# Kernel tuning notes

Measured on AMD Instinct MI355X. Metric: run time of the kernel, lower is better.

The kernel has to match this reference:

```python
import jax, jax.numpy as jnp
import numpy as np

B, T, D = 2, 2048, 2048
H, HKV = 16, 16
SEM, GEO = 1024, 1024
DH = D // H          # 128, v head dim
DS = SEM // H        # 64, sem head dim
DG = GEO // H        # 64, geo head dim (== rope_dim)
ROPE_BASE = 10000.0


def _split_heads(x, n_heads, hd):
    b, t, _ = x.shape
    return x.reshape(b, t, n_heads, hd).transpose(0, 2, 1, 3)  # (B,H,T,hd)


def _rope(x, pos_offset):
    # x: (B,H,T,DG); rotate-half RoPE over the full geo head dim
    b, h, t, d = x.shape
    inv_freq = 1.0 / (ROPE_BASE ** (jnp.arange(0, d, 2, dtype=jnp.float32) / d))
    pos = jnp.arange(t, dtype=jnp.float32) + jnp.float32(pos_offset)
    ang = pos[:, None] * inv_freq[None, :]            # (T, d/2)
    cos, sin = jnp.cos(ang), jnp.sin(ang)             # (T, d/2)
    x1, x2 = x[..., : d // 2], x[..., d // 2 :]
    return jnp.concatenate([x1 * cos - x2 * sin, x2 * cos + x1 * sin], axis=-1)


def setup_inputs() -> dict:
    key = jax.random.key(0)
    ks = jax.random.split(key, 8)
    s = lambda fan_in: 1.0 / np.sqrt(fan_in)
    return {
        "x": jax.random.normal(ks[0], (B, T, D), dtype=jnp.float32),
        "Wq_sem": jax.random.normal(ks[1], (D, SEM), dtype=jnp.float32) * s(D),
        "Wk_sem": jax.random.normal(ks[2], (D, SEM), dtype=jnp.float32) * s(D),
        "Wq_geo": jax.random.normal(ks[3], (D, GEO), dtype=jnp.float32) * s(D),
        "Wk_geo": jax.random.normal(ks[4], (D, GEO), dtype=jnp.float32) * s(D),
        "Wv": jax.random.normal(ks[5], (D, D), dtype=jnp.float32) * s(D),
        "Wo": jax.random.normal(ks[6], (D, D), dtype=jnp.float32) * s(D),
        "gate_logit": jax.random.normal(ks[7], (H,), dtype=jnp.float32) * 0.1,
        "pos_offset": 0,
    }


def reference(x, Wq_sem, Wk_sem, Wq_geo, Wk_geo, Wv, Wo, gate_logit, pos_offset):
    qsh = _split_heads(x @ Wq_sem, H, DS)    # (B,H,T,DS)
    ksh = _split_heads(x @ Wk_sem, HKV, DS)
    qgh = _split_heads(x @ Wq_geo, H, DG)    # (B,H,T,DG)
    kgh = _split_heads(x @ Wk_geo, HKV, DG)
    vh = _split_heads(x @ Wv, HKV, DH)       # (B,H,T,DH)

    qgh = _rope(qgh, pos_offset)
    kgh = _rope(kgh, pos_offset)

    gate = jax.nn.sigmoid(gate_logit).reshape(1, H, 1, 1).astype(x.dtype)
    qsh = qsh * (2.0 * gate)
    qgh = qgh * (2.0 - 2.0 * gate)

    sem_scale = 1.0 / np.sqrt(float(DS))
    geo_scale = 1.0 / np.sqrt(float(DG))
    # decoupled logits: sem and geo contributions each with their own scale
    logits = (jnp.einsum("bhqd,bhkd->bhqk", qsh, ksh) * sem_scale
              + jnp.einsum("bhqd,bhkd->bhqk", qgh, kgh) * geo_scale)

    t = x.shape[1]
    causal = jnp.tril(jnp.ones((t, t), dtype=bool))
    logits = jnp.where(causal, logits, jnp.finfo(logits.dtype).min)
    attn = jax.nn.softmax(logits, axis=-1)

    out_h = jnp.einsum("bhqk,bhkd->bhqd", attn, vh)   # (B,H,T,DH)
    out = out_h.transpose(0, 2, 1, 3).reshape(x.shape[0], t, H * DH)
    return out @ Wo
```

## Files before the change

### kernel.cpp

```cpp
#include <hip/hip_runtime.h>
#include <hip/hip_bf16.h>
#include <math.h>

#define B_ 2
#define T_ 2048
#define D_ 2048
#define H_ 16
#define DH_ 128
#define SEM_ 1024
#define GEO_ 1024
#define NPROJ 6144

typedef unsigned short ushort_t;
typedef short bf16x8 __attribute__((ext_vector_type(8)));
typedef float f32x4 __attribute__((ext_vector_type(4)));
typedef unsigned short us4 __attribute__((ext_vector_type(4)));

static __device__ inline ushort_t f2b(float x) {
    __hip_bfloat16 h = __float2bfloat16(x);
    return *reinterpret_cast<ushort_t*>(&h);
}
static __device__ inline float b2f(ushort_t u) {
    union { unsigned int i; float f; } v; v.i = ((unsigned int)u) << 16; return v.f;
}
static __device__ inline void gload_lds16(const ushort_t* g, ushort_t* l) {
    __builtin_amdgcn_global_load_lds(
        (const __attribute__((address_space(1))) void*)g,
        (__attribute__((address_space(3))) void*)l, 16, 0, 0);
}

__global__ __launch_bounds__(256) void convert_x(
    const float* __restrict__ x, ushort_t* __restrict__ xh)
{
    size_t i = ((size_t)blockIdx.x * 256 + threadIdx.x) * 8;
    float4 a = *(const float4*)&x[i];
    float4 b = *(const float4*)&x[i + 4];
    bf16x8 o;
    o[0] = (short)f2b(a.x); o[1] = (short)f2b(a.y);
    o[2] = (short)f2b(a.z); o[3] = (short)f2b(a.w);
    o[4] = (short)f2b(b.x); o[5] = (short)f2b(b.y);
    o[6] = (short)f2b(b.z); o[7] = (short)f2b(b.w);
    *(bf16x8*)&xh[i] = o;
}

__global__ __launch_bounds__(256) void transpose_all(
    const float* __restrict__ W0, const float* __restrict__ W1,
    const float* __restrict__ W2, const float* __restrict__ W3,
    const float* __restrict__ W4, const float* __restrict__ W5,
    ushort_t* __restrict__ Wt_all, ushort_t* __restrict__ WoT)
{
    const int z = blockIdx.z;
    const float* W;
    ushort_t* dst;
    int N;
    switch (z) {
        case 0: W = W0; dst = Wt_all;                          N = 1024; break;
        case 1: W = W1; dst = Wt_all + (size_t)1024 * 2048;    N = 1024; break;
        case 2: W = W2; dst = Wt_all + (size_t)2048 * 2048;    N = 1024; break;
        case 3: W = W3; dst = Wt_all + (size_t)3072 * 2048;    N = 1024; break;
        case 4: W = W4; dst = Wt_all + (size_t)4096 * 2048;    N = 2048; break;
        default: W = W5; dst = WoT;                            N = 2048; break;
    }
    const int n0 = blockIdx.x * 32;
    if (n0 >= N) return;
    const int k0 = blockIdx.y * 32;

    __shared__ float tile[32][33];
    const int c = threadIdx.x & 31, r = threadIdx.x >> 5;
#pragma unroll
    for (int rr = 0; rr < 32; rr += 8)
        tile[r + rr][c] = W[(size_t)(k0 + r + rr) * N + n0 + c];
    __syncthreads();
#pragma unroll
    for (int rr = 0; rr < 32; rr += 8)
        dst[(size_t)(n0 + r + rr) * 2048 + k0 + c] = f2b(tile[c][r + rr]);
}

#define BARS()  { asm volatile("" ::: "memory"); __builtin_amdgcn_s_barrier(); asm volatile("" ::: "memory"); }
#define WL0()   asm volatile("s_waitcnt lgkmcnt(0)" ::: "memory")
#define WV6()   asm volatile("s_waitcnt vmcnt(6)" ::: "memory")

#define LDA8(par, iq, i4, kk) \
    (*(const bf16x8*)&smA[(par)*16384 + (iq)*8192 + aoff + (i4)*1024 + ((kk) ? ca1 : ca0)])
#define LDB8(par, jq, j1, kk) \
    (*(const bf16x8*)&smB[(par)*16384 + (jq)*8192 + boff + (j1)*2048 + ((kk) ? ca1 : ca0)])

#define READ_A(par, iq) \
    aF[0]=LDA8(par,iq,0,0); aF[1]=LDA8(par,iq,0,1); \
    aF[2]=LDA8(par,iq,1,0); aF[3]=LDA8(par,iq,1,1); \
    aF[4]=LDA8(par,iq,2,0); aF[5]=LDA8(par,iq,2,1); \
    aF[6]=LDA8(par,iq,3,0); aF[7]=LDA8(par,iq,3,1);

#define READ_B(par, jq) \
    bF[(jq)*4+0]=LDB8(par,jq,0,0); bF[(jq)*4+1]=LDB8(par,jq,0,1); \
    bF[(jq)*4+2]=LDB8(par,jq,1,0); bF[(jq)*4+3]=LDB8(par,jq,1,1);

#define STAGE_A(h, kt, par) do { \
    const ushort_t* _s = gAbase + (size_t)((h)*128) * 2048 + (kt)*64 + stgoff; \
    ushort_t* _d = smA + (par)*16384 + (h)*8192 + wid*512; \
    gload_lds16(_s, _d); \
    gload_lds16(_s + (size_t)64*2048, _d + 4096); \
} while(0)

#define STAGE_B(h, kt, par) do { \
    const ushort_t* _s = gBbase + (size_t)((h)*128) * 2048 + (kt)*64 + stgoff; \
    ushort_t* _d = smB + (par)*16384 + (h)*8192 + wid*512; \
    gload_lds16(_s, _d); \
    gload_lds16(_s + (size_t)64*2048, _d + 4096); \
} while(0)

#define MM16(iq, jq) do { \
    _Pragma("unroll") \
    for (int i4 = 0; i4 < 4; ++i4) { \
        acc[(iq)*4+i4][(jq)*2+0] = __builtin_amdgcn_mfma_f32_16x16x32_bf16(aF[i4*2+0], bF[(jq)*4+0], acc[(iq)*4+i4][(jq)*2+0], 0, 0, 0); \
        acc[(iq)*4+i4][(jq)*2+0] = __builtin_amdgcn_mfma_f32_16x16x32_bf16(aF[i4*2+1], bF[(jq)*4+1], acc[(iq)*4+i4][(jq)*2+0], 0, 0, 0); \
        acc[(iq)*4+i4][(jq)*2+1] = __builtin_amdgcn_mfma_f32_16x16x32_bf16(aF[i4*2+0], bF[(jq)*4+2], acc[(iq)*4+i4][(jq)*2+1], 0, 0, 0); \
        acc[(iq)*4+i4][(jq)*2+1] = __builtin_amdgcn_mfma_f32_16x16x32_bf16(aF[i4*2+1], bF[(jq)*4+3], acc[(iq)*4+i4][(jq)*2+1], 0, 0, 0); \
    } \
} while(0)

#define TILE_BODY(par, parn, kt1, kt2) \
    STAGE_A(1, kt1, parn); \
    BARS(); WL0(); \
    __builtin_amdgcn_s_setprio(1); MM16(0, 0); __builtin_amdgcn_s_setprio(0); \
    READ_B(par, 1); \
    BARS(); \
    STAGE_A(0, kt2, par); \
    BARS(); WL0(); \
    __builtin_amdgcn_s_setprio(1); MM16(0, 1); __builtin_amdgcn_s_setprio(0); \
    READ_A(par, 1); \
    BARS(); \
    STAGE_B(0, kt2, par); \
    BARS(); WL0(); \
    __builtin_amdgcn_s_setprio(1); MM16(1, 1); __builtin_amdgcn_s_setprio(0); \
    BARS(); \
    STAGE_B(1, kt2, par); WV6(); \
    BARS(); \
    __builtin_amdgcn_s_setprio(1); MM16(1, 0); __builtin_amdgcn_s_setprio(0); \
    READ_A(parn, 0); READ_B(parn, 0); \
    BARS();

__global__ __launch_bounds__(512, 2) void gemm_proj(
    const ushort_t* __restrict__ A, const ushort_t* __restrict__ Bt,
    const float* __restrict__ gate_logit, const int* __restrict__ pos_off,
    ushort_t* __restrict__ Qh, ushort_t* __restrict__ Kh,
    ushort_t* __restrict__ Vt)
{
    extern __shared__ __align__(16) ushort_t smdyn[];
    ushort_t* smA = smdyn;
    ushort_t* smB = smdyn + 32768;

    const int tid  = threadIdx.x;
    const int wid  = tid >> 6, lane = tid & 63;
    const int ln16 = lane & 15, g = lane >> 4;
    const int wm = wid & 1, wn = wid >> 1;

    const int lin = blockIdx.y * 24 + blockIdx.x;
    const int swz = (lin & 7) * 48 + (lin >> 3);
    const int m0 = (swz / 24) * 256, n0 = (swz % 24) * 256;

    const int srow = wid * 8 + (lane >> 3);
    const int scol = ((lane & 7) ^ (lane >> 3)) * 8;
    const size_t stgoff = (size_t)srow * 2048 + scol;
    const ushort_t* gAbase = A  + (size_t)m0 * 2048;
    const ushort_t* gBbase = Bt + (size_t)n0 * 2048;

    const int cg0 = ln16 & 7;
    const int ca0 = ((g + 0) ^ cg0) * 8;
    const int ca1 = ((g + 4) ^ cg0) * 8;
    const int aoff = wm * 4096 + ln16 * 64;
    const int boff = (wn >> 1) * 4096 + (wn & 1) * 1024 + ln16 * 64;

    f32x4 acc[8][4];
#pragma unroll
    for (int i = 0; i < 8; ++i)
#pragma unroll
        for (int j = 0; j < 4; ++j) acc[i][j] = (f32x4){0.f, 0.f, 0.f, 0.f};
    bf16x8 aF[8], bF[8];

    STAGE_A(0, 0, 0); STAGE_B(0, 0, 0); STAGE_B(1, 0, 0); STAGE_A(1, 0, 0);
    STAGE_A(0, 1, 1); STAGE_B(0, 1, 1); STAGE_B(1, 1, 1);
    WV6();
    BARS();
    READ_A(0, 0); READ_B(0, 0);

#pragma unroll 1
    for (int t = 0; t < 32; t += 2) {
        const int ka1 = t + 1;
        const int ka2 = (t + 2 < 32) ? t + 2 : 31;
        const int kb1 = ka2;
        const int kb2 = (t + 3 < 32) ? t + 3 : 31;
        TILE_BODY(0, 1, ka1, ka2);
        TILE_BODY(1, 0, kb1, kb2);
    }
    asm volatile("s_waitcnt vmcnt(0) lgkmcnt(0)" ::: "memory");

    const int region = n0 >> 10;
    const int rbase  = m0 + wm * 64 + g * 4;

    if (region <= 1) {
        ushort_t* dst = (region == 0) ? Qh : Kh;
        const int hb  = ((n0 & 1023) >> 6) + (wn >> 1);
        const int d64 = (wn & 1) * 16 + ln16;
        float sc0 = 1.0f, sc1 = 1.0f;
        if (region == 0) {
            sc0 = 0.25f / (1.0f + __expf(-gate_logit[hb]));
            sc1 = 0.25f / (1.0f + __expf(-gate_logit[hb + 2]));
        }
#pragma unroll
        for (int i = 0; i < 8; ++i)
#pragma unroll
            for (int r = 0; r < 4; ++r) {
                int row = rbase + (i >> 2) * 128 + (i & 3) * 16 + r;
                int t = row & (T_ - 1), bb = row >> 11;
                size_t b0 = ((size_t)(bb * H_ + hb)     * T_ + t) * 128;
                size_t b1 = ((size_t)(bb * H_ + hb + 2) * T_ + t) * 128;
                dst[b0 + d64]      = f2b(acc[i][0][r] * sc0);
                dst[b0 + d64 + 32] = f2b(acc[i][1][r] * sc0);
                dst[b1 + d64]      = f2b(acc[i][2][r] * sc1);
                dst[b1 + d64 + 32] = f2b(acc[i][3][r] * sc1);
            }
    } else if (region <= 3) {
        ushort_t* dst = (region == 2) ? Qh : Kh;
        const int hb = ((n0 & 1023) >> 6) + (wn >> 1);
        const int ip = (wn & 1) * 16 + ln16;
        const float invf = __expf(-0.28782313665087625f * (float)ip);
        const float po = (float)(*pos_off);
        float sc0 = 1.0f, sc1 = 1.0f;
        if (region == 2) {
            sc0 = 0.25f * (1.0f - 1.0f / (1.0f + __expf(-gate_logit[hb])));
            sc1 = 0.25f * (1.0f - 1.0f / (1.0f + __expf(-gate_logit[hb + 2])));
        }
#pragma unroll
        for (int i = 0; i < 8; ++i)
#pragma unroll
            for (int r = 0; r < 4; ++r) {
                int row = rbase + (i >> 2) * 128 + (i & 3) * 16 + r;
                int t = row & (T_ - 1), bb = row >> 11;
                float s, c;
                __sincosf(((float)t + po) * invf, &s, &c);
                size_t b0 = ((size_t)(bb * H_ + hb)     * T_ + t) * 128;
                size_t b1 = ((size_t)(bb * H_ + hb + 2) * T_ + t) * 128;
                float x1 = acc[i][0][r], x2 = acc[i][1][r];
                dst[b0 + 64 + ip] = f2b((x1 * c - x2 * s) * sc0);
                dst[b0 + 96 + ip] = f2b((x2 * c + x1 * s) * sc0);
                x1 = acc[i][2][r]; x2 = acc[i][3][r];
                dst[b1 + 64 + ip] = f2b((x1 * c - x2 * s) * sc1);
                dst[b1 + 96 + ip] = f2b((x2 * c + x1 * s) * sc1);
            }
    } else {
        const int hb = (n0 - 4096) >> 7;
        const int db = (wn >> 1) * 64 + (wn & 1) * 16 + ln16;
#pragma unroll
        for (int i = 0; i < 8; ++i) {
            int row0 = rbase + (i >> 2) * 128 + (i & 3) * 16;
            int t0 = row0 & (T_ - 1), bb = row0 >> 11;
#pragma unroll
            for (int j = 0; j < 4; ++j) {
                us4 v;
                v[0] = f2b(acc[i][j][0]); v[1] = f2b(acc[i][j][1]);
                v[2] = f2b(acc[i][j][2]); v[3] = f2b(acc[i][j][3]);
                int hh = hb + (j >> 1);
                int dd = db + (j & 1) * 32;
                *(us4*)&Vt[((size_t)(bb * H_ + hh) * DH_ + dd) * T_ + t0] = v;
            }
        }
    }
}

__global__ __launch_bounds__(256) void gemm_bt_f32(
    const ushort_t* __restrict__ A, const ushort_t* __restrict__ Bt,
    float* __restrict__ C, int M, int N, int K)
{
    __shared__ ushort_t As[128 * 32];
    __shared__ ushort_t Bs[128 * 32];

    const int tid  = threadIdx.x;
    const int wid  = tid >> 6, lane = tid & 63;
    const int ln16 = lane & 15, g = lane >> 4;
    const int wm = wid & 1, wn = wid >> 1;
    const int m0 = blockIdx.y * 128, n0 = blockIdx.x * 128;

    const int lrow = lane >> 2;
    const int lc8  = (lane & 3) * 8;
    const ushort_t* gA = A  + (size_t)(m0 + wid * 32 + lrow) * K + lc8;
    const ushort_t* gB = Bt + (size_t)(n0 + wid * 32 + lrow) * K + lc8;
    ushort_t* lA = As + wid * 1024;
    ushort_t* lB = Bs + wid * 1024;
    const size_t K16 = (size_t)16 * K;

    f32x4 acc[4][4];
#pragma unroll
    for (int i = 0; i < 4; ++i)
#pragma unroll
        for (int j = 0; j < 4; ++j) acc[i][j] = (f32x4){0.f, 0.f, 0.f, 0.f};

    for (int k0 = 0; k0 < K; k0 += 32) {
        __syncthreads();
        gload_lds16(gA,       lA);
        gload_lds16(gA + K16, lA + 512);
        gload_lds16(gB,       lB);
        gload_lds16(gB + K16, lB + 512);
        gA += 32; gB += 32;
        __syncthreads();

        bf16x8 af[4], bfr[4];
#pragma unroll
        for (int i = 0; i < 4; ++i)
            af[i] = *(const bf16x8*)&As[(wm * 64 + i * 16 + ln16) * 32 + g * 8];
#pragma unroll
        for (int j = 0; j < 4; ++j)
            bfr[j] = *(const bf16x8*)&Bs[(wn * 64 + j * 16 + ln16) * 32 + g * 8];
#pragma unroll
        for (int i = 0; i < 4; ++i)
#pragma unroll
            for (int j = 0; j < 4; ++j)
                acc[i][j] = __builtin_amdgcn_mfma_f32_16x16x32_bf16(
                    af[i], bfr[j], acc[i][j], 0, 0, 0);
    }

#pragma unroll
    for (int i = 0; i < 4; ++i)
#pragma unroll
        for (int j = 0; j < 4; ++j)
#pragma unroll
            for (int r = 0; r < 4; ++r) {
                int row = m0 + wm * 64 + i * 16 + g * 4 + r;
                int col = n0 + wn * 64 + j * 16 + ln16;
                C[(size_t)row * N + col] = acc[i][j][r];
            }
}

#define P_PITCH  40

__global__ __launch_bounds__(256) void flash_attn(
    const ushort_t* __restrict__ Qh,
    const ushort_t* __restrict__ Kh,
    const ushort_t* __restrict__ Vt,
    ushort_t* __restrict__ aoh)
{
    __shared__ ushort_t Ks[32 * 128];
    __shared__ ushort_t Vs[128 * 32];
    __shared__ ushort_t Pl[4 * 16 * P_PITCH];

    const int tid  = threadIdx.x;
    const int wid  = tid >> 6, lane = tid & 63;
    const int ln16 = lane & 15, g = lane >> 4;
    const int p    = blockIdx.x;
    const int h  = blockIdx.y, b = blockIdx.z;
    const int bh = b * H_ + h;

    const ushort_t* Kbase = Kh + (size_t)bh * T_ * 128;
    const ushort_t* Vbase = Vt + (size_t)bh * 128 * T_;
    ushort_t* Pw = Pl + wid * 16 * P_PITCH;

    const int sk0 = tid,      sk1 = 256 + tid;
    const int kr0 = sk0 >> 4, kc0 = sk0 & 15;
    const int kr1 = sk1 >> 4, kc1 = sk1 & 15;
    const int vd0 = sk0 >> 2, vg0 = sk0 & 3;
    const int vd1 = sk1 >> 2, vg1 = sk1 & 3;
    const int kofs0 = (kc0 ^ (kr0 & 15)) * 8, kofs1 = (kc1 ^ (kr1 & 15)) * 8;
    const int vofs0 = (vg0 ^ ((vd0 + (vd0 >> 2)) & 3)) * 8;
    const int vofs1 = (vg1 ^ ((vd1 + (vd1 >> 2)) & 3)) * 8;

    bf16x8 bones;
    {
        short o = (ln16 == 0) ? (short)0x3F80 : (short)0;
#pragma unroll
        for (int j = 0; j < 8; ++j) bones[j] = o;
    }

#pragma unroll 1
    for (int ti = 0; ti < 2; ++ti) {
        const int qt = ti ? (31 - p) : p;
        const int q0 = qt * 64;
        const int qw = q0 + wid * 16;

        bf16x8 aq[4];
        {
            const ushort_t* qrow = Qh + ((size_t)bh * T_ + qw + ln16) * 128;
#pragma unroll
            for (int c2 = 0; c2 < 4; ++c2)
                aq[c2] = *(const bf16x8*)(qrow + c2 * 32 + g * 8);
        }

        f32x4 acc[8];
#pragma unroll
        for (int i = 0; i < 8; ++i) acc[i] = (f32x4){0.f, 0.f, 0.f, 0.f};
        f32x4 acc_l = (f32x4){0.f, 0.f, 0.f, 0.f};

        const int nkb  = q0 / 32 + 2;
        const int qmax = qw + 15;

        for (int kb = 0; kb < nkb; ++kb) {
            const int kt = kb * 32;
            __syncthreads();
            gload_lds16(Kbase + (size_t)(kt + kr0) * 128 + kofs0, Ks + wid * 512);
            gload_lds16(Kbase + (size_t)(kt + kr1) * 128 + kofs1, Ks + 2048 + wid * 512);
            gload_lds16(Vbase + (size_t)vd0 * T_ + kt + vofs0,    Vs + wid * 512);
            gload_lds16(Vbase + (size_t)vd1 * T_ + kt + vofs1,    Vs + 2048 + wid * 512);
            __syncthreads();
            if (kt > qmax) continue;

            f32x4 s0 = (f32x4){0.f, 0.f, 0.f, 0.f};
            f32x4 s1 = (f32x4){0.f, 0.f, 0.f, 0.f};
#pragma unroll
            for (int c2 = 0; c2 < 4; ++c2) {
                int jk = c2 * 4 + g;
                bf16x8 bk0 = *(const bf16x8*)&Ks[(ln16 * 16 + (jk ^ ln16)) * 8];
                bf16x8 bk1 = *(const bf16x8*)&Ks[(256 + ln16 * 16 + (jk ^ ln16)) * 8];
                s0 = __builtin_amdgcn_mfma_f32_16x16x32_bf16(aq[c2], bk0, s0, 0, 0, 0);
                s1 = __builtin_amdgcn_mfma_f32_16x16x32_bf16(aq[c2], bk1, s1, 0, 0, 0);
            }

            const bool diag = (kt + 31 > qw);
#pragma unroll
            for (int r2 = 0; r2 < 4; ++r2) {
                float e0 = __expf(s0[r2] - 12.0f);
                float e1 = __expf(s1[r2] - 12.0f);
                if (diag) {
                    int qr = qw + g * 4 + r2;
                    e0 = (kt + ln16      > qr) ? 0.0f : e0;
                    e1 = (kt + 16 + ln16 > qr) ? 0.0f : e1;
                }
                int prow = g * 4 + r2;
                Pw[prow * P_PITCH + ln16]      = f2b(e0);
                Pw[prow * P_PITCH + 16 + ln16] = f2b(e1);
            }
            __asm__ volatile("s_waitcnt lgkmcnt(0)" ::: "memory");
            bf16x8 ap = *(const bf16x8*)&Pw[ln16 * P_PITCH + g * 8];

#pragma unroll
            for (int cdv = 0; cdv < 8; ++cdv) {
                int d = cdv * 16 + ln16;
                bf16x8 bv = *(const bf16x8*)
                    &Vs[((d << 2) + (g ^ ((d + (d >> 2)) & 3))) * 8];
                acc[cdv] = __builtin_amdgcn_mfma_f32_16x16x32_bf16(ap, bv, acc[cdv], 0, 0, 0);
            }
            acc_l = __builtin_amdgcn_mfma_f32_16x16x32_bf16(ap, bones, acc_l, 0, 0, 0);
        }

        float invl[4];
#pragma unroll
        for (int r2 = 0; r2 < 4; ++r2)
            invl[r2] = 1.0f / __shfl(acc_l[r2], lane & 48);
#pragma unroll
        for (int cdv = 0; cdv < 8; ++cdv)
#pragma unroll
            for (int r2 = 0; r2 < 4; ++r2) {
                int qr = qw + g * 4 + r2;
                aoh[((size_t)b * T_ + qr) * D_ + h * DH_ + cdv * 16 + ln16] =
                    f2b(acc[cdv][r2] * invl[r2]);
            }
    }
}

extern "C" void kernel_launch(void* const* d_in, const int* in_sizes, int n_in,
                              void* d_out, int out_size, void* d_ws, size_t ws_size,
                              hipStream_t stream)
{
    const float* x       = (const float*)d_in[0];
    const float* Wq_sem  = (const float*)d_in[1];
    const float* Wk_sem  = (const float*)d_in[2];
    const float* Wq_geo  = (const float*)d_in[3];
    const float* Wk_geo  = (const float*)d_in[4];
    const float* Wv      = (const float*)d_in[5];
    const float* Wo      = (const float*)d_in[6];
    const float* gate    = (const float*)d_in[7];
    const int*   pos_off = (const int*)d_in[8];
    float* out = (float*)d_out;

    const int M = B_ * T_;
    char* ws = (char*)d_ws;
    ushort_t* xh     = (ushort_t*)(ws);
    ushort_t* aoh    = xh;
    ushort_t* Wt_all = (ushort_t*)(ws + (size_t)16 * 1048576);
    ushort_t* WoT    = (ushort_t*)(ws + (size_t)40 * 1048576);
    ushort_t* Qh     = (ushort_t*)(ws + (size_t)48 * 1048576);
    ushort_t* Kh     = (ushort_t*)(ws + (size_t)64 * 1048576);
    ushort_t* Vt     = (ushort_t*)(ws + (size_t)80 * 1048576);

    dim3 blk(256);

    convert_x<<<(M * D_) / (256 * 8), blk, 0, stream>>>(x, xh);
    transpose_all<<<dim3(64, 64, 6), blk, 0, stream>>>(
        Wq_sem, Wk_sem, Wq_geo, Wk_geo, Wv, Wo, Wt_all, WoT);

    hipFuncSetAttribute((const void*)gemm_proj,
                        hipFuncAttributeMaxDynamicSharedMemorySize, 131072);
    gemm_proj<<<dim3(NPROJ / 256, M / 256), dim3(512), 131072, stream>>>(
        xh, Wt_all, gate, pos_off, Qh, Kh, Vt);

    flash_attn<<<dim3(16, H_, B_), blk, 0, stream>>>(Qh, Kh, Vt, aoh);

    gemm_bt_f32<<<dim3(D_ / 128, M / 128), blk, 0, stream>>>(
        aoh, WoT, out, M, D_, D_);
}
```

Baseline: 397.9 us.

## Load K/V fragments directly from global into registers, drop LDS staging

The flash attention kernel no longer stages K and V tiles through shared memory with block-wide barriers. Each wave now loads its own K and V MFMA fragments straight from global memory into registers, prefetches the next K block, bounds the loop per wave by its own causal limit, and raises wave priority around the MFMAs. The projection GEMM's tile-swizzle mapping is also removed in favour of a plain block-index mapping. This removes the barriers and LDS traffic, but each of the four waves now fetches the same K/V data from global memory separately, relying on cache for reuse, and the GEMM loses its cache-locality ordering.

```diff
diff --git a/kernel.cpp b/kernel.cpp
--- a/kernel.cpp
+++ b/kernel.cpp
@@ -154,10 +154,7 @@
     const int wid  = tid >> 6, lane = tid & 63;
     const int ln16 = lane & 15, g = lane >> 4;
     const int wm = wid & 1, wn = wid >> 1;
-
-    const int lin = blockIdx.y * 24 + blockIdx.x;
-    const int swz = (lin & 7) * 48 + (lin >> 3);
-    const int m0 = (swz / 24) * 256, n0 = (swz % 24) * 256;
+    const int m0 = blockIdx.y * 256, n0 = blockIdx.x * 256;
 
     const int srow = wid * 8 + (lane >> 3);
     const int scol = ((lane & 7) ^ (lane >> 3)) * 8;
@@ -339,8 +336,6 @@
     const ushort_t* __restrict__ Vt,
     ushort_t* __restrict__ aoh)
 {
-    __shared__ ushort_t Ks[32 * 128];
-    __shared__ ushort_t Vs[128 * 32];
     __shared__ ushort_t Pl[4 * 16 * P_PITCH];
 
     const int tid  = threadIdx.x;
@@ -354,14 +349,9 @@
     const ushort_t* Vbase = Vt + (size_t)bh * 128 * T_;
     ushort_t* Pw = Pl + wid * 16 * P_PITCH;
 
-    const int sk0 = tid,      sk1 = 256 + tid;
-    const int kr0 = sk0 >> 4, kc0 = sk0 & 15;
-    const int kr1 = sk1 >> 4, kc1 = sk1 & 15;
-    const int vd0 = sk0 >> 2, vg0 = sk0 & 3;
-    const int vd1 = sk1 >> 2, vg1 = sk1 & 3;
-    const int kofs0 = (kc0 ^ (kr0 & 15)) * 8, kofs1 = (kc1 ^ (kr1 & 15)) * 8;
-    const int vofs0 = (vg0 ^ ((vd0 + (vd0 >> 2)) & 3)) * 8;
-    const int vofs1 = (vg1 ^ ((vd1 + (vd1 >> 2)) & 3)) * 8;
+    const ushort_t* K0p = Kbase + (size_t)ln16 * 128 + g * 8;
+    const ushort_t* K1p = K0p + 16 * 128;
+    const ushort_t* Vp  = Vbase + (size_t)ln16 * T_ + g * 8;
 
     bf16x8 bones;
     {
@@ -389,29 +379,44 @@
         for (int i = 0; i < 8; ++i) acc[i] = (f32x4){0.f, 0.f, 0.f, 0.f};
         f32x4 acc_l = (f32x4){0.f, 0.f, 0.f, 0.f};
 
-        const int nkb  = q0 / 32 + 2;
         const int qmax = qw + 15;
-
-        for (int kb = 0; kb < nkb; ++kb) {
+        const int kbw  = qmax >> 5;
+
+        bf16x8 kA0[4], kA1[4];
+#pragma unroll
+        for (int c2 = 0; c2 < 4; ++c2) {
+            kA0[c2] = *(const bf16x8*)(K0p + c2 * 32);
+            kA1[c2] = *(const bf16x8*)(K1p + c2 * 32);
+        }
+
+#pragma unroll 1
+        for (int kb = 0; kb <= kbw; ++kb) {
             const int kt = kb * 32;
-            __syncthreads();
-            gload_lds16(Kbase + (size_t)(kt + kr0) * 128 + kofs0, Ks + wid * 512);
-            gload_lds16(Kbase + (size_t)(kt + kr1) * 128 + kofs1, Ks + 2048 + wid * 512);
-            gload_lds16(Vbase + (size_t)vd0 * T_ + kt + vofs0,    Vs + wid * 512);
-            gload_lds16(Vbase + (size_t)vd1 * T_ + kt + vofs1,    Vs + 2048 + wid * 512);
-            __syncthreads();
-            if (kt > qmax) continue;
+
+            bf16x8 bv[8];
+#pragma unroll
+            for (int cdv = 0; cdv < 8; ++cdv)
+                bv[cdv] = *(const bf16x8*)(Vp + (size_t)(cdv * 16) * T_ + kt);
+
+            bf16x8 kN0[4], kN1[4];
+            if (kb < kbw) {
+                const size_t ko = (size_t)(kt + 32) * 128;
+#pragma unroll
+                for (int c2 = 0; c2 < 4; ++c2) {
+                    kN0[c2] = *(const bf16x8*)(K0p + ko + c2 * 32);
+                    kN1[c2] = *(const bf16x8*)(K1p + ko + c2 * 32);
+                }
+            }
 
             f32x4 s0 = (f32x4){0.f, 0.f, 0.f, 0.f};
             f32x4 s1 = (f32x4){0.f, 0.f, 0.f, 0.f};
+            __builtin_amdgcn_s_setprio(1);
 #pragma unroll
             for (int c2 = 0; c2 < 4; ++c2) {
-                int jk = c2 * 4 + g;
-                bf16x8 bk0 = *(const bf16x8*)&Ks[(ln16 * 16 + (jk ^ ln16)) * 8];
-                bf16x8 bk1 = *(const bf16x8*)&Ks[(256 + ln16 * 16 + (jk ^ ln16)) * 8];
-                s0 = __builtin_amdgcn_mfma_f32_16x16x32_bf16(aq[c2], bk0, s0, 0, 0, 0);
-                s1 = __builtin_amdgcn_mfma_f32_16x16x32_bf16(aq[c2], bk1, s1, 0, 0, 0);
-            }
+                s0 = __builtin_amdgcn_mfma_f32_16x16x32_bf16(aq[c2], kA0[c2], s0, 0, 0, 0);
+                s1 = __builtin_amdgcn_mfma_f32_16x16x32_bf16(aq[c2], kA1[c2], s1, 0, 0, 0);
+            }
+            __builtin_amdgcn_s_setprio(0);
 
             const bool diag = (kt + 31 > qw);
 #pragma unroll
@@ -430,14 +435,20 @@
             __asm__ volatile("s_waitcnt lgkmcnt(0)" ::: "memory");
             bf16x8 ap = *(const bf16x8*)&Pw[ln16 * P_PITCH + g * 8];
 
-#pragma unroll
-            for (int cdv = 0; cdv < 8; ++cdv) {
-                int d = cdv * 16 + ln16;
-                bf16x8 bv = *(const bf16x8*)
-                    &Vs[((d << 2) + (g ^ ((d + (d >> 2)) & 3))) * 8];
-                acc[cdv] = __builtin_amdgcn_mfma_f32_16x16x32_bf16(ap, bv, acc[cdv], 0, 0, 0);
-            }
+            __builtin_amdgcn_s_setprio(1);
+#pragma unroll
+            for (int cdv = 0; cdv < 8; ++cdv)
+                acc[cdv] = __builtin_amdgcn_mfma_f32_16x16x32_bf16(ap, bv[cdv], acc[cdv], 0, 0, 0);
             acc_l = __builtin_amdgcn_mfma_f32_16x16x32_bf16(ap, bones, acc_l, 0, 0, 0);
+            __builtin_amdgcn_s_setprio(0);
+
+            if (kb < kbw) {
+#pragma unroll
+                for (int c2 = 0; c2 < 4; ++c2) {
+                    kA0[c2] = kN0[c2];
+                    kA1[c2] = kN1[c2];
+                }
+            }
         }
 
         float invl[4];
```

Measured after the change: 533.9 us. +34.2%, slower.

## Double-buffer K/V tiles in flash attention and reorder block mapping

Applied to the files above, without the earlier changes.

Flash attention now keeps two LDS buffers for K and V. The next tile's global-to-LDS load is issued before computing the current tile, so memory latency overlaps with MFMA work, and each iteration needs only one barrier instead of two. MFMA sections are wrapped in s_setprio, and the block index is linearized so heads and batches of the same query pair are adjacent. The projection GEMM drops its swizzled tile mapping and goes back to a plain row-major block order, which may reduce L2 reuse. Double buffering doubles the K/V LDS footprint.

```diff
diff --git a/kernel.cpp b/kernel.cpp
--- a/kernel.cpp
+++ b/kernel.cpp
@@ -154,10 +154,7 @@
     const int wid  = tid >> 6, lane = tid & 63;
     const int ln16 = lane & 15, g = lane >> 4;
     const int wm = wid & 1, wn = wid >> 1;
-
-    const int lin = blockIdx.y * 24 + blockIdx.x;
-    const int swz = (lin & 7) * 48 + (lin >> 3);
-    const int m0 = (swz / 24) * 256, n0 = (swz % 24) * 256;
+    const int m0 = blockIdx.y * 256, n0 = blockIdx.x * 256;
 
     const int srow = wid * 8 + (lane >> 3);
     const int scol = ((lane & 7) ^ (lane >> 3)) * 8;
@@ -333,21 +330,31 @@
 
 #define P_PITCH  40
 
+#define FA_STAGE(kt, buf) do { \
+    gload_lds16(Kbase + (size_t)((kt) + kr0) * 128 + kofs0, Ks + (buf)*4096 + wid * 512); \
+    gload_lds16(Kbase + (size_t)((kt) + kr1) * 128 + kofs1, Ks + (buf)*4096 + 2048 + wid * 512); \
+    gload_lds16(Vbase + (size_t)vd0 * T_ + (kt) + vofs0,    Vs + (buf)*4096 + wid * 512); \
+    gload_lds16(Vbase + (size_t)vd1 * T_ + (kt) + vofs1,    Vs + (buf)*4096 + 2048 + wid * 512); \
+} while(0)
+
 __global__ __launch_bounds__(256) void flash_attn(
     const ushort_t* __restrict__ Qh,
     const ushort_t* __restrict__ Kh,
     const ushort_t* __restrict__ Vt,
     ushort_t* __restrict__ aoh)
 {
-    __shared__ ushort_t Ks[32 * 128];
-    __shared__ ushort_t Vs[128 * 32];
+    __shared__ ushort_t Ks[2 * 32 * 128];
+    __shared__ ushort_t Vs[2 * 128 * 32];
     __shared__ ushort_t Pl[4 * 16 * P_PITCH];
 
     const int tid  = threadIdx.x;
     const int wid  = tid >> 6, lane = tid & 63;
     const int ln16 = lane & 15, g = lane >> 4;
-    const int p    = blockIdx.x;
-    const int h  = blockIdx.y, b = blockIdx.z;
+
+    const int lin = blockIdx.x + (blockIdx.y << 4) + (blockIdx.z << 8);
+    const int h = lin & 15;
+    const int b = (lin >> 4) & 1;
+    const int p = lin >> 5;
     const int bh = b * H_ + h;
 
     const ushort_t* Kbase = Kh + (size_t)bh * T_ * 128;
@@ -392,52 +399,62 @@
         const int nkb  = q0 / 32 + 2;
         const int qmax = qw + 15;
 
+        FA_STAGE(0, 0);
+        asm volatile("s_waitcnt vmcnt(0)" ::: "memory");
+        BARS();
+
+#pragma unroll 1
         for (int kb = 0; kb < nkb; ++kb) {
             const int kt = kb * 32;
-            __syncthreads();
-            gload_lds16(Kbase + (size_t)(kt + kr0) * 128 + kofs0, Ks + wid * 512);
-            gload_lds16(Kbase + (size_t)(kt + kr1) * 128 + kofs1, Ks + 2048 + wid * 512);
-            gload_lds16(Vbase + (size_t)vd0 * T_ + kt + vofs0,    Vs + wid * 512);
-            gload_lds16(Vbase + (size_t)vd1 * T_ + kt + vofs1,    Vs + 2048 + wid * 512);
-            __syncthreads();
-            if (kt > qmax) continue;
-
-            f32x4 s0 = (f32x4){0.f, 0.f, 0.f, 0.f};
-            f32x4 s1 = (f32x4){0.f, 0.f, 0.f, 0.f};
-#pragma unroll
-            for (int c2 = 0; c2 < 4; ++c2) {
-                int jk = c2 * 4 + g;
-                bf16x8 bk0 = *(const bf16x8*)&Ks[(ln16 * 16 + (jk ^ ln16)) * 8];
-                bf16x8 bk1 = *(const bf16x8*)&Ks[(256 + ln16 * 16 + (jk ^ ln16)) * 8];
-                s0 = __builtin_amdgcn_mfma_f32_16x16x32_bf16(aq[c2], bk0, s0, 0, 0, 0);
-                s1 = __builtin_amdgcn_mfma_f32_16x16x32_bf16(aq[c2], bk1, s1, 0, 0, 0);
+            if (kb + 1 < nkb) FA_STAGE(kt + 32, (kb + 1) & 1);
+
+            if (kt <= qmax) {
+                const int kbuf = (kb & 1) * 4096;
+
+                f32x4 s0 = (f32x4){0.f, 0.f, 0.f, 0.f};
+                f32x4 s1 = (f32x4){0.f, 0.f, 0.f, 0.f};
+                __builtin_amdgcn_s_setprio(1);
+#pragma unroll
+                for (int c2 = 0; c2 < 4; ++c2) {
+                    int jk = c2 * 4 + g;
+                    bf16x8 bk0 = *(const bf16x8*)&Ks[kbuf + (ln16 * 16 + (jk ^ ln16)) * 8];
+                    bf16x8 bk1 = *(const bf16x8*)&Ks[kbuf + (256 + ln16 * 16 + (jk ^ ln16)) * 8];
+                    s0 = __builtin_amdgcn_mfma_f32_16x16x32_bf16(aq[c2], bk0, s0, 0, 0, 0);
+                    s1 = __builtin_amdgcn_mfma_f32_16x16x32_bf16(aq[c2], bk1, s1, 0, 0, 0);
+                }
+                __builtin_amdgcn_s_setprio(0);
+
+                const bool diag = (kt + 31 > qw);
+#pragma unroll
+                for (int r2 = 0; r2 < 4; ++r2) {
+                    float e0 = __expf(s0[r2] - 12.0f);
+                    float e1 = __expf(s1[r2] - 12.0f);
+                    if (diag) {
+                        int qr = qw + g * 4 + r2;
+                        e0 = (kt + ln16      > qr) ? 0.0f : e0;
+                        e1 = (kt + 16 + ln16 > qr) ? 0.0f : e1;
+                    }
+                    int prow = g * 4 + r2;
+                    Pw[prow * P_PITCH + ln16]      = f2b(e0);
+                    Pw[prow * P_PITCH + 16 + ln16] = f2b(e1);
+                }
+                __asm__ volatile("s_waitcnt lgkmcnt(0)" ::: "memory");
+                bf16x8 ap = *(const bf16x8*)&Pw[ln16 * P_PITCH + g * 8];
+
+                __builtin_amdgcn_s_setprio(1);
+#pragma unroll
+                for (int cdv = 0; cdv < 8; ++cdv) {
+                    int d = cdv * 16 + ln16;
+                    bf16x8 bv = *(const bf16x8*)
+                        &Vs[kbuf + ((d << 2) + (g ^ ((d + (d >> 2)) & 3))) * 8];
+                    acc[cdv] = __builtin_amdgcn_mfma_f32_16x16x32_bf16(ap, bv, acc[cdv], 0, 0, 0);
+                }
+                acc_l = __builtin_amdgcn_mfma_f32_16x16x32_bf16(ap, bones, acc_l, 0, 0, 0);
+                __builtin_amdgcn_s_setprio(0);
             }
 
-            const bool diag = (kt + 31 > qw);
-#pragma unroll
-            for (int r2 = 0; r2 < 4; ++r2) {
-                float e0 = __expf(s0[r2] - 12.0f);
-                float e1 = __expf(s1[r2] - 12.0f);
-                if (diag) {
-                    int qr = qw + g * 4 + r2;
-                    e0 = (kt + ln16      > qr) ? 0.0f : e0;
-                    e1 = (kt + 16 + ln16 > qr) ? 0.0f : e1;
-                }
-                int prow = g * 4 + r2;
-                Pw[prow * P_PITCH + ln16]      = f2b(e0);
-                Pw[prow * P_PITCH + 16 + ln16] = f2b(e1);
-            }
-            __asm__ volatile("s_waitcnt lgkmcnt(0)" ::: "memory");
-            bf16x8 ap = *(const bf16x8*)&Pw[ln16 * P_PITCH + g * 8];
-
-#pragma unroll
-            for (int cdv = 0; cdv < 8; ++cdv) {
-                int d = cdv * 16 + ln16;
-                bf16x8 bv = *(const bf16x8*)
-                    &Vs[((d << 2) + (g ^ ((d + (d >> 2)) & 3))) * 8];
-                acc[cdv] = __builtin_amdgcn_mfma_f32_16x16x32_bf16(ap, bv, acc[cdv], 0, 0, 0);
-            }
-            acc_l = __builtin_amdgcn_mfma_f32_16x16x32_bf16(ap, bones, acc_l, 0, 0, 0);
+            asm volatile("s_waitcnt vmcnt(0)" ::: "memory");
+            BARS();
         }
 
         float invl[4];
```

Result: no change. 391.1 us (-1.7%).
